# Kernel tuning notes

Hardware: AMD Instinct MI355X
Metric: run time of the kernel (lower is better)

Reference implementation:

```python
import jax, jax.numpy as jnp
import numpy as np

N = 100000   # nodes
E = 1600000  # edges (before self-loops)
G = 128      # graphs in batch
IN = 128     # in_channels
H = 64       # GCN hidden dim
OUT = 7      # out_channels
N_STACK = 9  # 64->64 GCN layers after the first


def setup_inputs() -> dict:
    key = jax.random.key(0)
    ks = jax.random.split(key, 10)
    s = 0.1
    x = jax.random.normal(ks[0], (N, IN), dtype=jnp.float32)
    edge_index = jax.random.randint(ks[1], (2, E), 0, N, dtype=jnp.int32)
    batch = jnp.sort(jax.random.randint(ks[2], (N,), 0, G, dtype=jnp.int32))
    W0 = jax.random.normal(ks[3], (IN, H), dtype=jnp.float32) * s
    b0 = jnp.zeros((H,), dtype=jnp.float32)
    Ws = jax.random.normal(ks[4], (N_STACK, H, H), dtype=jnp.float32) * s
    bs = jnp.zeros((N_STACK, H), dtype=jnp.float32)
    Wlin = jax.random.normal(ks[5], (H, OUT), dtype=jnp.float32) * s
    blin = jnp.zeros((OUT,), dtype=jnp.float32)
    return {"x": x, "edge_index": edge_index, "batch": batch,
            "W0": W0, "b0": b0, "Ws": Ws, "bs": bs,
            "Wlin": Wlin, "blin": blin}


def reference(x, edge_index, batch, W0, b0, Ws, bs, Wlin, blin):
    # GCNConv with add_self_loops=True, normalize=True (PyG defaults):
    # out = D^{-1/2} (A + I) D^{-1/2} (X W) + b
    loop = jnp.arange(N, dtype=edge_index.dtype)
    src = jnp.concatenate([edge_index[0], loop])   # [E+N]
    dst = jnp.concatenate([edge_index[1], loop])   # [E+N]
    ones = jnp.ones_like(dst, dtype=x.dtype)
    deg = jax.ops.segment_sum(ones, dst, num_segments=N)       # in-degree incl. self-loop
    dinv = jnp.where(deg > 0, jax.lax.rsqrt(deg), 0.0)
    norm = dinv[src] * dinv[dst]                                # [E+N]

    def gcn(h, W, b):
        m = h @ W                                               # [N,H] linear first
        agg = jax.ops.segment_sum(norm[:, None] * m[src], dst, num_segments=N)
        return agg + b

    h = jax.nn.relu(gcn(x, W0, b0))
    # nn.Dropout / EvalDropout are identity in the deterministic reference

    def step(h, wb):
        W, b = wb
        return jax.nn.relu(gcn(h, W, b)), None

    h, _ = jax.lax.scan(step, h, (Ws, bs))                      # 9 stacked GCN layers

    # global_mean_pool over graph ids
    counts = jax.ops.segment_sum(jnp.ones((N,), dtype=h.dtype), batch, num_segments=G)
    pooled = jax.ops.segment_sum(h, batch, num_segments=G) / jnp.clip(counts, 1.0)[:, None]
    return pooled @ Wlin + blin                                 # [G, OUT]
```

## Files before the change

### kernel.cpp

```cpp
#include <hip/hip_runtime.h>
#include <hip/hip_fp16.h>

#define NNODES 100000
#define NEDGES 1600000
#define NGRAPH 128
#define CIN 128
#define CH 64
#define COUT 7
#define NSTACK 9

#define NB 391
#define CHUNK 2048
#define NC 782

template <int K>
__global__ __launch_bounds__(256) void hist_gemm_kernel(const int* __restrict__ dst,
                                                        int* __restrict__ hist, int E,
                                                        const float* __restrict__ h,
                                                        const float* __restrict__ W,
                                                        __half* __restrict__ m, int N,
                                                        int histBlocks) {
    __shared__ float Ws[K * 64];
    __shared__ int lh[NB];
    if (blockIdx.x < (unsigned)histBlocks) {
        for (int i = threadIdx.x; i < NB; i += 256) lh[i] = 0;
        __syncthreads();
        int e0 = blockIdx.x * CHUNK;
        int e1 = min(e0 + CHUNK, E);
        for (int e = e0 + threadIdx.x; e < e1; e += 256)
            atomicAdd(&lh[dst[e] >> 8], 1);
        __syncthreads();
        for (int i = threadIdx.x; i < NB; i += 256) hist[i * NC + (int)blockIdx.x] = lh[i];
        return;
    }
    int gb = blockIdx.x - histBlocks;
    for (int i = threadIdx.x; i < K * 64; i += 256) Ws[i] = W[i];
    __syncthreads();
    const int ROWS = 8;
    int wid = __builtin_amdgcn_readfirstlane((gb * 256 + (int)threadIdx.x) >> 6);
    int lane = threadIdx.x & 63;
    long row0 = (long)wid * ROWS;
    if (row0 >= N) return;
    const float* __restrict__ hr = h + row0 * K;

    float acc[ROWS];
#pragma unroll
    for (int r = 0; r < ROWS; ++r) acc[r] = 0.0f;

    for (int k0 = 0; k0 < K; k0 += 4) {
        float wv[4];
#pragma unroll
        for (int j = 0; j < 4; ++j) wv[j] = Ws[(k0 + j) * 64 + lane];
#pragma unroll
        for (int r = 0; r < ROWS; ++r) {
#pragma unroll
            for (int j = 0; j < 4; ++j)
                acc[r] += hr[(size_t)r * K + k0 + j] * wv[j];
        }
    }

    __half* mo = m + row0 * 64 + lane;
#pragma unroll
    for (int r = 0; r < ROWS; ++r) mo[r * 64] = __float2half(acc[r]);
}

__global__ __launch_bounds__(256) void scan_chunks_kernel(int* __restrict__ hist,
                                                          int* __restrict__ btot) {
    int b = blockIdx.x;
    int t = threadIdx.x;
    int* row = hist + b * NC;
    int v[4];
    int base = 4 * t;
#pragma unroll
    for (int u = 0; u < 4; ++u) v[u] = (base + u < NC) ? row[base + u] : 0;
    int tsum = v[0] + v[1] + v[2] + v[3];
    __shared__ int s[256];
    s[t] = tsum;
    __syncthreads();
    for (int d = 1; d < 256; d <<= 1) {
        int x = (t >= d) ? s[t - d] : 0;
        __syncthreads();
        s[t] += x;
        __syncthreads();
    }
    int run = s[t] - tsum;
    if (t == 255) btot[b] = s[255];
#pragma unroll
    for (int u = 0; u < 4; ++u) {
        if (base + u < NC) row[base + u] = run;
        run += v[u];
    }
}

__global__ void scan_buckets_kernel(const int* __restrict__ tot, int* __restrict__ out) {
    __shared__ int s[512];
    int t = threadIdx.x;
    int v = (t < NB) ? tot[t] : 0;
    s[t] = v;
    __syncthreads();
    for (int d = 1; d < 512; d <<= 1) {
        int x = (t >= d) ? s[t - d] : 0;
        __syncthreads();
        s[t] += x;
        __syncthreads();
    }
    if (t < NB) out[t] = s[t] - v;
    if (t == NB - 1) out[NB] = s[t];
}

__global__ __launch_bounds__(256) void scatter_kernel(const int* __restrict__ src,
                                                      const int* __restrict__ dst,
                                                      const int* __restrict__ hist,
                                                      const int* __restrict__ bbase,
                                                      int* __restrict__ src_b,
                                                      int* __restrict__ dst_b, int E) {
    __shared__ int offs[NB];
    for (int b = threadIdx.x; b < NB; b += 256)
        offs[b] = hist[b * NC + (int)blockIdx.x] + bbase[b];
    __syncthreads();
    int e0 = blockIdx.x * CHUNK;
    int e1 = min(e0 + CHUNK, E);
    for (int e = e0 + threadIdx.x; e < e1; e += 256) {
        int d = dst[e], s = src[e];
        int pos = atomicAdd(&offs[d >> 8], 1);
        src_b[pos] = s;
        dst_b[pos] = d;
    }
}

__global__ __launch_bounds__(256) void bucket_prep_kernel(const int* __restrict__ dst_b,
                                                          const int* __restrict__ bbase,
                                                          const int* __restrict__ btot,
                                                          int* __restrict__ rowptr,
                                                          int* __restrict__ pbt,
                                                          float* __restrict__ dinv,
                                                          const int* __restrict__ batch,
                                                          int* __restrict__ gcnt, int N) {
    if ((int)blockIdx.x == NB) {
        int g = threadIdx.x;
        if (g >= NGRAPH) return;
        auto lb = [&](int v) {
            int lo = 0, hi = N;
            while (lo < hi) {
                int mid = (lo + hi) >> 1;
                if (batch[mid] < v) lo = mid + 1; else hi = mid;
            }
            return lo;
        };
        gcnt[g] = lb(g + 1) - lb(g);
        return;
    }
    __shared__ int c256[256];
    __shared__ int s[256];
    int t = threadIdx.x;
    c256[t] = 0;
    __syncthreads();
    int lo = bbase[blockIdx.x], n = btot[blockIdx.x];
    for (int e = lo + t; e < lo + n; e += 256) atomicAdd(&c256[dst_b[e] & 255], 1);
    __syncthreads();
    int cnt = c256[t];
    int pcnt = (cnt + 7) & ~7;
    s[t] = pcnt;
    __syncthreads();
    for (int d = 1; d < 256; d <<= 1) {
        int x = (t >= d) ? s[t - d] : 0;
        __syncthreads();
        s[t] += x;
        __syncthreads();
    }
    int node = blockIdx.x * 256 + t;
    if (node < N) {
        rowptr[node] = s[t] - pcnt;
        dinv[node] = 1.0f / sqrtf((float)(cnt + 1));
    }
    if (t == 255) pbt[blockIdx.x] = s[255];
}

__global__ void rowptr_fix_kernel(int* __restrict__ rowptr, const int* __restrict__ pbbase,
                                  int N) {
    int i = blockIdx.x * 256 + threadIdx.x;
    if (i < N) rowptr[i] += pbbase[i >> 8];
    if (i == 0) rowptr[N] = pbbase[NB];
}

__global__ __launch_bounds__(256) void bucket_fill_kernel(const int* __restrict__ src_b,
                                                          const int* __restrict__ dst_b,
                                                          const int* __restrict__ bbase,
                                                          const int* __restrict__ btot,
                                                          const int* __restrict__ rowptr,
                                                          int* __restrict__ col, int N) {
    __shared__ int f256[256];
    __shared__ int rp[256];
    int t = threadIdx.x;
    f256[t] = 0;
    int node = blockIdx.x * 256 + t;
    rp[t] = (node < N) ? rowptr[node] : 0;
    __syncthreads();
    int lo = bbase[blockIdx.x], n = btot[blockIdx.x];
    for (int e = lo + t; e < lo + n; e += 256) {
        int d = dst_b[e], sv = src_b[e];
        int li = d & 255;
        int slot = atomicAdd(&f256[li], 1);
        col[rp[li] + slot] = sv;
    }
    __syncthreads();
    if (node < N) {
        int c = f256[t];
        int pc = (c + 7) & ~7;
        int base = rp[t];
        for (int p = c; p < pc; ++p) col[base + p] = N;
    }
}

__global__ __launch_bounds__(256) void scale_m_kernel(__half* __restrict__ m,
                                                      __half* __restrict__ other,
                                                      const float* __restrict__ dinv, int N) {
    if (blockIdx.x == 0 && threadIdx.x < 64) {
        m[(size_t)N * 64 + threadIdx.x] = __float2half(0.0f);
        other[(size_t)N * 64 + threadIdx.x] = __float2half(0.0f);
    }
    int tot = N * 32;
    __half2* m2 = (__half2*)m;
    for (int idx = blockIdx.x * 256 + threadIdx.x; idx < tot; idx += gridDim.x * 256) {
        float d = dinv[idx >> 5];
        float2 f = __half22float2(m2[idx]);
        f.x *= d;
        f.y *= d;
        m2[idx] = __float22half2_rn(f);
    }
}

__device__ __forceinline__ void pair_gather(const __half* __restrict__ h,
                                            const int* __restrict__ col,
                                            int r0, int mid, int r1, int lane,
                                            float& aA, float& aB) {
    int n = r1 - r0;
    int e = 0;
    for (; e + 16 <= n; e += 16) {
        int base = r0 + e;
        int c[16];
        float v[16];
#pragma unroll
        for (int u = 0; u < 16; ++u) c[u] = col[base + u];
#pragma unroll
        for (int u = 0; u < 16; ++u) v[u] = __half2float(h[(size_t)c[u] * 64 + lane]);
        float s0 = ((v[0] + v[1]) + (v[2] + v[3])) + ((v[4] + v[5]) + (v[6] + v[7]));
        float s1 = ((v[8] + v[9]) + (v[10] + v[11])) + ((v[12] + v[13]) + (v[14] + v[15]));
        bool b0 = (base < mid);
        bool b1 = (base + 8 < mid);
        aA += b0 ? s0 : 0.0f;
        aB += b0 ? 0.0f : s0;
        aA += b1 ? s1 : 0.0f;
        aB += b1 ? 0.0f : s1;
    }
    if (e + 8 <= n) {
        int base = r0 + e;
        int c[8];
        float v[8];
#pragma unroll
        for (int u = 0; u < 8; ++u) c[u] = col[base + u];
#pragma unroll
        for (int u = 0; u < 8; ++u) v[u] = __half2float(h[(size_t)c[u] * 64 + lane]);
        float s0 = ((v[0] + v[1]) + (v[2] + v[3])) + ((v[4] + v[5]) + (v[6] + v[7]));
        bool b0 = (base < mid);
        aA += b0 ? s0 : 0.0f;
        aB += b0 ? 0.0f : s0;
    }
}

__global__ __launch_bounds__(256) void agg0_kernel(const __half* __restrict__ m,
                                                   const int* __restrict__ rowptr,
                                                   const int* __restrict__ col,
                                                   const float* __restrict__ dinv,
                                                   const float* __restrict__ bias,
                                                   __half* __restrict__ hout, int N) {
    int wid = __builtin_amdgcn_readfirstlane((blockIdx.x * 256 + threadIdx.x) >> 6);
    int lane = threadIdx.x & 63;
    int nodeA = wid * 2;
    int nodeB = nodeA + 1;
    if (nodeA >= N) return;
    int r0 = rowptr[nodeA];
    int mid = rowptr[nodeB];
    int r1 = rowptr[nodeB + 1];
    float diA = dinv[nodeA], diB = dinv[nodeB];
    float aA = __half2float(m[(size_t)nodeA * 64 + lane]);
    float aB = __half2float(m[(size_t)nodeB * 64 + lane]);
    pair_gather(m, col, r0, mid, r1, lane, aA, aB);
    float bv = bias[lane];
    float hA = fmaxf(diA * aA + bv, 0.0f);
    float hB = fmaxf(diB * aB + bv, 0.0f);
    hout[(size_t)nodeA * 64 + lane] = __float2half(diA * hA);
    hout[(size_t)nodeB * 64 + lane] = __float2half(diB * hB);
}

__global__ __launch_bounds__(256) void fused_kernel(const __half* __restrict__ h,
                                                    const int* __restrict__ rowptr,
                                                    const int* __restrict__ col,
                                                    const float* __restrict__ dinv,
                                                    const float* __restrict__ W,
                                                    const float* __restrict__ bias,
                                                    __half* __restrict__ hout, int N,
                                                    int scaleOut) {
    __shared__ float Ws[64 * 64];
    {
        const float4* W4 = (const float4*)W;
        float4* Ws4 = (float4*)Ws;
        for (int i = threadIdx.x; i < 64 * 16; i += 256) Ws4[i] = W4[i];
    }

    int wid = __builtin_amdgcn_readfirstlane((blockIdx.x * 256 + threadIdx.x) >> 6);
    int lane = threadIdx.x & 63;
    int nodeA = wid * 2;
    int nodeB = nodeA + 1;
    bool act = (nodeA < N);
    float gA = 0.0f, gB = 0.0f;
    float diA = 0.0f, diB = 0.0f;

    if (act) {
        int r0 = rowptr[nodeA];
        int mid = rowptr[nodeB];
        int r1 = rowptr[nodeB + 1];
        diA = dinv[nodeA];
        diB = dinv[nodeB];
        float aA = __half2float(h[(size_t)nodeA * 64 + lane]);
        float aB = __half2float(h[(size_t)nodeB * 64 + lane]);
        pair_gather(h, col, r0, mid, r1, lane, aA, aB);
        gA = diA * aA;
        gB = diB * aB;
    }

    __syncthreads();

    if (act) {
        float bv = bias[lane];
        float accA = bv, accB = bv;
#pragma unroll
        for (int k = 0; k < 64; ++k) {
            float wv = Ws[k * 64 + lane];
            unsigned ga = __builtin_amdgcn_readlane(__float_as_uint(gA), k);
            unsigned gb = __builtin_amdgcn_readlane(__float_as_uint(gB), k);
            accA += __uint_as_float(ga) * wv;
            accB += __uint_as_float(gb) * wv;
        }
        accA = fmaxf(accA, 0.0f);
        accB = fmaxf(accB, 0.0f);
        if (scaleOut) { accA *= diA; accB *= diB; }
        hout[(size_t)nodeA * 64 + lane] = __float2half(accA);
        hout[(size_t)nodeB * 64 + lane] = __float2half(accB);
    }
}

__global__ __launch_bounds__(256) void pool_kernel(const __half* __restrict__ h,
                                                   const int* __restrict__ batch,
                                                   float* __restrict__ gpool, int N) {
    const int NPW = 32;
    int wid = (blockIdx.x * 256 + threadIdx.x) >> 6;
    int lane = threadIdx.x & 63;
    int i0 = wid * NPW;
    if (i0 >= N) return;
    int i1 = min(i0 + NPW, N);
    int curg = batch[i0];
    float acc = 0.0f;
    for (int i = i0; i < i1; ++i) {
        int g = batch[i];
        if (g != curg) {
            atomicAdd(&gpool[curg * 64 + lane], acc);
            acc = 0.0f;
            curg = g;
        }
        acc += __half2float(h[(size_t)i * 64 + lane]);
    }
    atomicAdd(&gpool[curg * 64 + lane], acc);
}

__global__ void final_kernel(const float* __restrict__ gpool, const int* __restrict__ gcnt,
                             const float* __restrict__ Wlin, const float* __restrict__ blin,
                             float* __restrict__ out) {
    int t = threadIdx.x;
    if (t >= NGRAPH * COUT) return;
    int g = t / COUT, o = t - g * COUT;
    float c = (float)gcnt[g];
    if (c < 1.0f) c = 1.0f;
    float s = 0.0f;
    for (int k = 0; k < 64; ++k) s += gpool[g * 64 + k] * Wlin[k * COUT + o];
    out[t] = s / c + blin[o];
}

extern "C" void kernel_launch(void* const* d_in, const int* in_sizes, int n_in,
                              void* d_out, int out_size, void* d_ws, size_t ws_size,
                              hipStream_t stream) {
    const float* x    = (const float*)d_in[0];
    const int*   ei   = (const int*)d_in[1];
    const int*   batch= (const int*)d_in[2];
    const float* W0   = (const float*)d_in[3];
    const float* b0   = (const float*)d_in[4];
    const float* Ws   = (const float*)d_in[5];
    const float* bs   = (const float*)d_in[6];
    const float* Wlin = (const float*)d_in[7];
    const float* blin = (const float*)d_in[8];
    float* out = (float*)d_out;

    const int N = NNODES, E = NEDGES;
    const int* srcp = ei;
    const int* dstp = ei + E;

    char* w = (char*)d_ws;
    float* gpool  = (float*)w; w += (size_t)NGRAPH * 64 * 4;
    size_t zero_bytes = (size_t)(w - (char*)d_ws);
    int*   gcnt   = (int*)w;   w += (size_t)NGRAPH * 4;
    float* dinv   = (float*)w; w += (size_t)N * 4;
    int*   rowptr = (int*)w;   w += (size_t)(N + 1) * 4;
    int*   hist   = (int*)w;   w += (size_t)NB * NC * 4;
    int*   btot   = (int*)w;   w += (size_t)NB * 4;
    int*   bbase  = (int*)w;   w += (size_t)(NB + 1) * 4;
    int*   pbt    = (int*)w;   w += (size_t)NB * 4;
    int*   pbbase = (int*)w;   w += (size_t)(NB + 1) * 4;
    int*   src_b  = (int*)w;   w += (size_t)E * 4;
    int*   dst_b  = (int*)w;   w += (size_t)E * 4;
    int*   col    = (int*)w;   w += ((size_t)E + 8 * N) * 4;
    __half* bufA  = (__half*)w; w += (size_t)(N + 1) * 64 * 2;
    __half* bufB  = (__half*)w; w += (size_t)(N + 1) * 64 * 2;

    hipMemsetAsync(d_ws, 0, zero_bytes, stream);

    int nblocks = (N + 255) / 256;
    int gemmblocks = (N + 31) / 32;

    hist_gemm_kernel<128><<<NC + gemmblocks, 256, 0, stream>>>(
        dstp, hist, E, x, W0, bufB, N, NC);
    scan_chunks_kernel<<<NB, 256, 0, stream>>>(hist, btot);
    scan_buckets_kernel<<<1, 512, 0, stream>>>(btot, bbase);
    scatter_kernel<<<NC, 256, 0, stream>>>(srcp, dstp, hist, bbase, src_b, dst_b, E);
    bucket_prep_kernel<<<NB + 1, 256, 0, stream>>>(dst_b, bbase, btot, rowptr, pbt, dinv,
                                                   batch, gcnt, N);
    scan_buckets_kernel<<<1, 512, 0, stream>>>(pbt, pbbase);
    rowptr_fix_kernel<<<nblocks, 256, 0, stream>>>(rowptr, pbbase, N);
    bucket_fill_kernel<<<NB, 256, 0, stream>>>(src_b, dst_b, bbase, btot, rowptr, col, N);
    scale_m_kernel<<<2048, 256, 0, stream>>>(bufB, bufA, dinv, N);

    int pairblocks = (N / 2 + 3) / 4;

    agg0_kernel<<<pairblocks, 256, 0, stream>>>(bufB, rowptr, col, dinv, b0, bufA, N);

    __half* hin = bufA;
    __half* hout = bufB;
    for (int l = 0; l < NSTACK; ++l) {
        int scaleOut = (l < NSTACK - 1) ? 1 : 0;
        fused_kernel<<<pairblocks, 256, 0, stream>>>(hin, rowptr, col, dinv,
                                                     Ws + (size_t)l * 64 * 64,
                                                     bs + (size_t)l * 64, hout, N,
                                                     scaleOut);
        __half* t = hin; hin = hout; hout = t;
    }

    int pwaves = (N + 31) / 32;
    int pblocks = (pwaves + 3) / 4;
    pool_kernel<<<pblocks, 256, 0, stream>>>(hin, batch, gpool, N);
    final_kernel<<<1, 896, 0, stream>>>(gpool, gcnt, Wlin, blin, out);
}
```

Before: 694.0 us.

## Compute first-layer 128->64 GEMM with split-bf16 MFMA instead of scalar FMAs

Replaces the scalar FP32 FMA loop in the fused histogram/GEMM kernel with MFMA 16x16x32 bf16 instructions. Each operand is split into bf16 hi and lo parts, and three MFMAs per tile keep accuracy close to FP32. W is pre-split into a fragment layout in shared memory, and each wave now handles 16 rows with vectorized float4 loads of x. The aim is to cut the ALU-bound cost of the first layer's linear transform, at the price of extra conversion work and a small loss of precision versus full FP32.

```diff
diff --git a/kernel.cpp b/kernel.cpp
--- a/kernel.cpp
+++ b/kernel.cpp
@@ -13,16 +13,23 @@
 #define CHUNK 2048
 #define NC 782
 
-template <int K>
+typedef __attribute__((ext_vector_type(8))) short bf16x8;
+typedef __attribute__((ext_vector_type(4))) float f32x4;
+
+__device__ __forceinline__ unsigned short f2bf(float f) {
+    unsigned u = __float_as_uint(f);
+    return (unsigned short)((u + 0x7FFFu + ((u >> 16) & 1u)) >> 16);
+}
+
 __global__ __launch_bounds__(256) void hist_gemm_kernel(const int* __restrict__ dst,
                                                         int* __restrict__ hist, int E,
                                                         const float* __restrict__ h,
                                                         const float* __restrict__ W,
                                                         __half* __restrict__ m, int N,
                                                         int histBlocks) {
-    __shared__ float Ws[K * 64];
-    __shared__ int lh[NB];
+    __shared__ alignas(16) char smem[32768 + 2048];
     if (blockIdx.x < (unsigned)histBlocks) {
+        int* lh = (int*)smem;
         for (int i = threadIdx.x; i < NB; i += 256) lh[i] = 0;
         __syncthreads();
         int e0 = blockIdx.x * CHUNK;
@@ -34,34 +41,71 @@
         return;
     }
     int gb = blockIdx.x - histBlocks;
-    for (int i = threadIdx.x; i < K * 64; i += 256) Ws[i] = W[i];
-    __syncthreads();
-    const int ROWS = 8;
-    int wid = __builtin_amdgcn_readfirstlane((gb * 256 + (int)threadIdx.x) >> 6);
-    int lane = threadIdx.x & 63;
-    long row0 = (long)wid * ROWS;
+    unsigned short* wf_hi = (unsigned short*)smem;
+    unsigned short* wf_lo = wf_hi + 16 * 64 * 8;
+    int t = threadIdx.x;
+
+    {
+        int c = t >> 4;
+        int kstep = c >> 2, ncol = c & 3;
+        int l0 = (t & 15) * 4;
+        for (int dl = 0; dl < 4; ++dl) {
+            int l = l0 + dl;
+            int kbase = kstep * 32 + (l >> 4) * 8;
+            int n = ncol * 16 + (l & 15);
+            for (int i = 0; i < 8; ++i) {
+                float wv = W[(size_t)(kbase + i) * 64 + n];
+                unsigned short hb = f2bf(wv);
+                float hf = __uint_as_float(((unsigned)hb) << 16);
+                wf_hi[((size_t)c * 64 + l) * 8 + i] = hb;
+                wf_lo[((size_t)c * 64 + l) * 8 + i] = f2bf(wv - hf);
+            }
+        }
+    }
+    __syncthreads();
+
+    int wave = t >> 6, lane = t & 63;
+    long row0 = (long)gb * 64 + wave * 16;
     if (row0 >= N) return;
-    const float* __restrict__ hr = h + row0 * K;
-
-    float acc[ROWS];
-#pragma unroll
-    for (int r = 0; r < ROWS; ++r) acc[r] = 0.0f;
-
-    for (int k0 = 0; k0 < K; k0 += 4) {
-        float wv[4];
-#pragma unroll
-        for (int j = 0; j < 4; ++j) wv[j] = Ws[(k0 + j) * 64 + lane];
-#pragma unroll
-        for (int r = 0; r < ROWS; ++r) {
-#pragma unroll
-            for (int j = 0; j < 4; ++j)
-                acc[r] += hr[(size_t)r * K + k0 + j] * wv[j];
+
+    long arow = row0 + (lane & 15);
+    const float4* xr = (const float4*)(h + (size_t)arow * 128);
+    int kg = lane >> 4;
+
+    f32x4 zero = {0.0f, 0.0f, 0.0f, 0.0f};
+    f32x4 acc[4];
+    acc[0] = zero; acc[1] = zero; acc[2] = zero; acc[3] = zero;
+
+#pragma unroll
+    for (int s = 0; s < 4; ++s) {
+        float4 p = xr[s * 8 + kg * 2];
+        float4 q = xr[s * 8 + kg * 2 + 1];
+        float xv[8] = {p.x, p.y, p.z, p.w, q.x, q.y, q.z, q.w};
+        bf16x8 a_hi, a_lo;
+#pragma unroll
+        for (int i = 0; i < 8; ++i) {
+            unsigned short hb = f2bf(xv[i]);
+            a_hi[i] = (short)hb;
+            a_lo[i] = (short)f2bf(xv[i] - __uint_as_float(((unsigned)hb) << 16));
         }
-    }
-
-    __half* mo = m + row0 * 64 + lane;
-#pragma unroll
-    for (int r = 0; r < ROWS; ++r) mo[r * 64] = __float2half(acc[r]);
+#pragma unroll
+        for (int nc = 0; nc < 4; ++nc) {
+            int c = s * 4 + nc;
+            bf16x8 b_hi = *(const bf16x8*)(wf_hi + ((size_t)c * 64 + lane) * 8);
+            bf16x8 b_lo = *(const bf16x8*)(wf_lo + ((size_t)c * 64 + lane) * 8);
+            acc[nc] = __builtin_amdgcn_mfma_f32_16x16x32_bf16(a_hi, b_hi, acc[nc], 0, 0, 0);
+            acc[nc] = __builtin_amdgcn_mfma_f32_16x16x32_bf16(a_hi, b_lo, acc[nc], 0, 0, 0);
+            acc[nc] = __builtin_amdgcn_mfma_f32_16x16x32_bf16(a_lo, b_hi, acc[nc], 0, 0, 0);
+        }
+    }
+
+    int drow = (lane >> 4) * 4;
+    int dcol = lane & 15;
+#pragma unroll
+    for (int nc = 0; nc < 4; ++nc)
+#pragma unroll
+        for (int r = 0; r < 4; ++r)
+            m[(size_t)(row0 + drow + r) * 64 + nc * 16 + dcol] = __float2half(acc[nc][r]);
 }
 
 __global__ __launch_bounds__(256) void scan_chunks_kernel(int* __restrict__ hist,
@@ -424,9 +468,9 @@
     hipMemsetAsync(d_ws, 0, zero_bytes, stream);
 
     int nblocks = (N + 255) / 256;
-    int gemmblocks = (N + 31) / 32;
-
-    hist_gemm_kernel<128><<<NC + gemmblocks, 256, 0, stream>>>(
+    int gemmblocks = (N + 63) / 64;
+
+    hist_gemm_kernel<<<NC + gemmblocks, 256, 0, stream>>>(
         dstp, hist, E, x, W0, bufB, N, NC);
     scan_chunks_kernel<<<NB, 256, 0, stream>>>(hist, btot);
     scan_buckets_kernel<<<1, 512, 0, stream>>>(btot, bbase);
```

Measured after the change: 650.7 us. 1.07x faster.
